# Kernel optimization log

Hardware: AMD Instinct MI355X
Metric: run time of the kernel (lower is better)

## Reference

```python
import jax, jax.numpy as jnp
import numpy as np

F_FRAMES = 128   # number of frames (seq_start_end rows)
P_PEDS = 32      # pedestrians per frame (uniform)
B = F_FRAMES * P_PEDS
E, H, BN, PM, M = 64, 128, 1024, 512, 1024
PRED_LEN = 12


def setup_inputs() -> dict:
    key = jax.random.key(0)
    ks = jax.random.split(key, 20)
    n = lambda k, s, sc=0.05: (jax.random.normal(k, s) * sc).astype(jnp.float32)
    starts = jnp.arange(F_FRAMES, dtype=jnp.int32) * P_PEDS
    seq_start_end = jnp.stack([starts, starts + P_PEDS], axis=1)
    return {
        "h0": n(ks[0], (1, B, H), 1.0),
        "c0": n(ks[1], (1, B, H), 1.0),
        "obs_final_pos": n(ks[2], (B, 2), 1.0),
        "obs_final_pos_rel": n(ks[3], (B, 2), 1.0),
        "W_emb": n(ks[4], (2, E)), "b_emb": jnp.zeros((E,), jnp.float32),
        "W_ih": n(ks[5], (4 * H, E)), "W_hh": n(ks[6], (4 * H, H)),
        "b_ih": jnp.zeros((4 * H,), jnp.float32), "b_hh": jnp.zeros((4 * H,), jnp.float32),
        "W_pos": n(ks[7], (H, 2)), "b_pos": jnp.zeros((2,), jnp.float32),
        "W_pe": n(ks[8], (2, E)), "b_pe": jnp.zeros((E,), jnp.float32),
        "W_p1": n(ks[9], (E + H, PM)), "b_p1": jnp.zeros((PM,), jnp.float32),
        "W_p2": n(ks[10], (PM, BN)), "b_p2": jnp.zeros((BN,), jnp.float32),
        "W_m1": n(ks[11], (H + BN, M)), "b_m1": jnp.zeros((M,), jnp.float32),
        "W_m2": n(ks[12], (M, H)), "b_m2": jnp.zeros((H,), jnp.float32),
        "seq_start_end": seq_start_end,
    }


def reference(h0, c0, obs_final_pos, obs_final_pos_rel,
              W_emb, b_emb, W_ih, W_hh, b_ih, b_hh, W_pos, b_pos,
              W_pe, b_pe, W_p1, b_p1, W_p2, b_p2, W_m1, b_m1, W_m2, b_m2,
              seq_start_end):
    Bn = h0.shape[1]
    F = seq_start_end.shape[0]
    P = Bn // F  # uniform frame size
    h, c = h0[0], c0[0]
    x0 = obs_final_pos_rel @ W_emb + b_emb  # decoder input embedding

    def step(carry, _):
        x, h, c, last_pos = carry
        # LSTM cell (PyTorch gate order i,f,g,o)
        gates = x @ W_ih.T + h @ W_hh.T + b_ih + b_hh  # (B, 4H)
        i, f, g, o = jnp.split(gates, 4, axis=-1)
        i, f, o = jax.nn.sigmoid(i), jax.nn.sigmoid(f), jax.nn.sigmoid(o)
        c_new = f * c + i * jnp.tanh(g)
        h_new = o * jnp.tanh(c_new)
        rel_pos = h_new @ W_pos + b_pos
        curr_pos = rel_pos + last_pos
        # PoolNet: per-frame pairwise rel-pos embed + MLP + max over neighbours j
        pos = curr_pos.reshape(F, P, 2)
        hf = h_new.reshape(F, P, H)
        rel = pos[:, None, :, :] - pos[:, :, None, :]  # rel[f,i,j] = pos_j - pos_i
        e = rel @ W_pe + b_pe  # (F,P,P,E)
        feat = jnp.concatenate(
            [e, jnp.broadcast_to(hf[:, None], (F, P, P, H))], axis=-1)  # h of j
        z = jax.nn.relu(feat @ W_p1 + b_p1)
        z = jax.nn.relu(z @ W_p2 + b_p2)  # (F,P,P,BN)
        pool_h = z.max(axis=2).reshape(Bn, BN)
        # hidden refresh MLP
        mi = jnp.concatenate([h_new, pool_h], axis=-1)
        nh = jax.nn.relu(mi @ W_m1 + b_m1)
        nh = jax.nn.relu(nh @ W_m2 + b_m2)
        x_new = rel_pos @ W_emb + b_emb
        return (x_new, nh, c_new, curr_pos), (curr_pos, rel_pos)

    _, (pred_seq, pred_seq_rel) = jax.lax.scan(
        jax.checkpoint(step), (x0, h, c, obs_final_pos), None, length=PRED_LEN)
    return pred_seq, pred_seq_rel
```

## Files before the change

### kernel.cpp

```cpp
#include <hip/hip_runtime.h>

#define NB 4096
#define HD 128
#define ED 64
#define NF 128
#define NP 32
#define TSTEPS 12

typedef __attribute__((ext_vector_type(8))) short short8;
typedef __attribute__((ext_vector_type(8))) __bf16 bf16x8;
typedef __attribute__((ext_vector_type(8))) _Float16 f16x8;
typedef __attribute__((ext_vector_type(4))) float f32x4;

#define MFMA16(a, b, c) __builtin_amdgcn_mfma_f32_16x16x32_bf16((a), (b), (c), 0, 0, 0)
#define MFMAH(a, b, c)  __builtin_amdgcn_mfma_f32_16x16x32_f16((a), (b), (c), 0, 0, 0)

__device__ __forceinline__ unsigned short f2bf(float f) {
  unsigned int x = __float_as_uint(f);
  x += 0x7fffu + ((x >> 16) & 1u);
  return (unsigned short)(x >> 16);
}

__device__ __forceinline__ float sigm(float x) { return 1.0f / (1.0f + expf(-x)); }

__device__ __forceinline__ f16x8 relu8(f16x8 x) {
  return __builtin_elementwise_max(x, (f16x8)(_Float16)0);
}


__global__ __launch_bounds__(256) void k_transpose_bf(const float* __restrict__ W,
                                                      unsigned short* __restrict__ Wt,
                                                      int K, int N) {
  __shared__ float t[32][33];
  int nb = blockIdx.x * 32, kb = blockIdx.y * 32;
  int tx = threadIdx.x & 31, ty = threadIdx.x >> 5;
  #pragma unroll
  for (int r = 0; r < 32; r += 8)
    t[ty + r][tx] = W[(size_t)(kb + ty + r) * N + nb + tx];
  __syncthreads();
  #pragma unroll
  for (int r = 0; r < 32; r += 8)
    Wt[(size_t)(nb + ty + r) * K + kb + tx] = f2bf(t[tx][ty + r]);
}

__global__ __launch_bounds__(256) void k_transpose_f16(const float* __restrict__ W,
                                                       _Float16* __restrict__ Wt,
                                                       int K, int N) {
  __shared__ float t[32][33];
  int nb = blockIdx.x * 32, kb = blockIdx.y * 32;
  int tx = threadIdx.x & 31, ty = threadIdx.x >> 5;
  #pragma unroll
  for (int r = 0; r < 32; r += 8)
    t[ty + r][tx] = W[(size_t)(kb + ty + r) * N + nb + tx];
  __syncthreads();
  #pragma unroll
  for (int r = 0; r < 32; r += 8)
    Wt[(size_t)(nb + ty + r) * K + kb + tx] = (_Float16)t[tx][ty + r];
}

__global__ __launch_bounds__(256) void k_pack_lstm_w(const float* __restrict__ Wih,
                                                     const float* __restrict__ Whh,
                                                     float* __restrict__ WihT,
                                                     float* __restrict__ WhhT) {
  int idx = blockIdx.x * 256 + threadIdx.x;
  if (idx < 64 * 512) { int k = idx >> 9, n = idx & 511; WihT[idx] = Wih[n * 64 + k]; }
  if (idx < 128 * 512) { int k = idx >> 9, n = idx & 511; WhhT[idx] = Whh[n * 128 + k]; }
}

__global__ __launch_bounds__(256) void k_pack_wpp(const float* __restrict__ Wpe,
                                                  const float* __restrict__ bpe,
                                                  const float* __restrict__ Wp1,
                                                  const float* __restrict__ bp1,
                                                  float* __restrict__ Wpp,
                                                  float* __restrict__ cvec) {
  int n = blockIdx.x * 256 + threadIdx.x;
  if (n >= 512) return;
  float s0 = 0.f, s1 = 0.f, sc = 0.f;
  for (int k = 0; k < 64; ++k) {
    float w = Wp1[k * 512 + n];
    s0 += Wpe[k] * w;
    s1 += Wpe[64 + k] * w;
    sc += bpe[k] * w;
  }
  Wpp[n * 2] = s0; Wpp[n * 2 + 1] = s1; cvec[n] = sc + bp1[n];
}

__global__ __launch_bounds__(256) void k_x0(const float* __restrict__ ofr,
                                            const float* __restrict__ Wemb,
                                            const float* __restrict__ bemb,
                                            float* __restrict__ x) {
  int idx = blockIdx.x * 256 + threadIdx.x;
  if (idx >= NB * ED) return;
  int row = idx >> 6, e = idx & 63;
  x[idx] = bemb[e] + ofr[row * 2] * Wemb[e] + ofr[row * 2 + 1] * Wemb[64 + e];
}


__global__ __launch_bounds__(256) void k12_lstm_uv(
    const float* __restrict__ x, const float* __restrict__ hin, const float* __restrict__ cin,
    const float* __restrict__ WihT, const float* __restrict__ WhhT,
    const float* __restrict__ bih, const float* __restrict__ bhh,
    const float* __restrict__ Wpos, const float* __restrict__ bpos,
    const float* __restrict__ Wemb, const float* __restrict__ bemb,
    const float* __restrict__ lastpos,
    const float* __restrict__ Wp1, const float* __restrict__ Wpp,
    const float* __restrict__ cvec,
    float* __restrict__ cout, unsigned short* __restrict__ mi,
    float* __restrict__ posout, float* __restrict__ xout,
    float* __restrict__ outc, float* __restrict__ outr,
    _Float16* __restrict__ u16, _Float16* __restrict__ v16) {
  __shared__ float xh[8][192];
  __shared__ float hnl[8][128];
  __shared__ float rp[8][2];
  __shared__ float cp[8][2];
  int tid = threadIdx.x;
  int r0 = blockIdx.x * 8;
  for (int idx = tid; idx < 8 * 192; idx += 256) {
    int r = idx / 192, k = idx % 192;
    xh[r][k] = (k < 64) ? x[(r0 + r) * 64 + k] : hin[(r0 + r) * 128 + (k - 64)];
  }
  __syncthreads();
  int j = tid & 127, rg = tid >> 7;
  float acc0[4], acc1[4], acc2[4], acc3[4];
  {
    float b0 = bih[j] + bhh[j];
    float b1 = bih[128 + j] + bhh[128 + j];
    float b2 = bih[256 + j] + bhh[256 + j];
    float b3 = bih[384 + j] + bhh[384 + j];
    #pragma unroll
    for (int r = 0; r < 4; ++r) { acc0[r] = b0; acc1[r] = b1; acc2[r] = b2; acc3[r] = b3; }
  }
  for (int k = 0; k < 64; ++k) {
    float w0 = WihT[k * 512 + j], w1 = WihT[k * 512 + 128 + j],
          w2 = WihT[k * 512 + 256 + j], w3 = WihT[k * 512 + 384 + j];
    #pragma unroll
    for (int r = 0; r < 4; ++r) {
      float xv = xh[rg * 4 + r][k];
      acc0[r] += w0 * xv; acc1[r] += w1 * xv; acc2[r] += w2 * xv; acc3[r] += w3 * xv;
    }
  }
  for (int k = 0; k < 128; ++k) {
    float w0 = WhhT[k * 512 + j], w1 = WhhT[k * 512 + 128 + j],
          w2 = WhhT[k * 512 + 256 + j], w3 = WhhT[k * 512 + 384 + j];
    #pragma unroll
    for (int r = 0; r < 4; ++r) {
      float hv = xh[rg * 4 + r][64 + k];
      acc0[r] += w0 * hv; acc1[r] += w1 * hv; acc2[r] += w2 * hv; acc3[r] += w3 * hv;
    }
  }
  #pragma unroll
  for (int r = 0; r < 4; ++r) {
    int row = r0 + rg * 4 + r;
    float ig = sigm(acc0[r]), fg = sigm(acc1[r]), gg = tanhf(acc2[r]), og = sigm(acc3[r]);
    float cn = fg * cin[row * 128 + j] + ig * gg;
    float hv = og * tanhf(cn);
    cout[row * 128 + j] = cn;
    mi[(size_t)row * 1152 + j] = f2bf(hv);
    hnl[rg * 4 + r][j] = hv;
  }
  __syncthreads();
  {
    int r = tid >> 5;
    int d = (tid >> 4) & 1;
    int l = tid & 15;
    float s = 0.f;
    #pragma unroll
    for (int k = l; k < 128; k += 16) s += hnl[r][k] * Wpos[k * 2 + d];
    s += __shfl_xor(s, 1);
    s += __shfl_xor(s, 2);
    s += __shfl_xor(s, 4);
    s += __shfl_xor(s, 8);
    if (l == 0) {
      int row = r0 + r;
      float rel = s + bpos[d];
      float cur = rel + lastpos[row * 2 + d];
      rp[r][d] = rel;
      cp[r][d] = cur;
      posout[row * 2 + d] = cur;
      outc[row * 2 + d] = cur;
      outr[row * 2 + d] = rel;
    }
  }
  __syncthreads();
  for (int idx = tid; idx < 8 * 64; idx += 256) {
    int r = idx >> 6, e = idx & 63;
    xout[(r0 + r) * 64 + e] = bemb[e] + rp[r][0] * Wemb[e] + rp[r][1] * Wemb[64 + e];
  }
  int n = tid, n2 = tid + 256;
  float aA[8], aB[8];
  #pragma unroll
  for (int r = 0; r < 8; ++r) { aA[r] = 0.f; aB[r] = 0.f; }
  for (int k = 0; k < 128; ++k) {
    float wA = Wp1[(64 + k) * 512 + n], wB = Wp1[(64 + k) * 512 + n2];
    #pragma unroll
    for (int r = 0; r < 8; ++r) { aA[r] += wA * hnl[r][k]; aB[r] += wB * hnl[r][k]; }
  }
  float wp0A = Wpp[n * 2], wp1A = Wpp[n * 2 + 1], cA = cvec[n];
  float wp0B = Wpp[n2 * 2], wp1B = Wpp[n2 * 2 + 1], cB = cvec[n2];
  #pragma unroll
  for (int r = 0; r < 8; ++r) {
    int row = r0 + r;
    float t0 = cp[r][0] * wp0A + cp[r][1] * wp1A;
    v16[(size_t)row * 512 + n] = (_Float16)t0;
    u16[(size_t)row * 512 + n] = (_Float16)(t0 + aA[r] + cA);
    float t1 = cp[r][0] * wp0B + cp[r][1] * wp1B;
    v16[(size_t)row * 512 + n2] = (_Float16)t1;
    u16[(size_t)row * 512 + n2] = (_Float16)(t1 + aB[r] + cB);
  }
}

__global__ __launch_bounds__(256, 2) void k3_pool(
    const _Float16* __restrict__ u16, const _Float16* __restrict__ v16,
    const _Float16* __restrict__ Bt, const float* __restrict__ bp2,
    unsigned short* __restrict__ mi) {
  __shared__ _Float16 v_lds[4 * 512];
  __shared__ _Float16 u_ch[2][32 * 32];
  __shared__ _Float16 b_ch[2][256 * 32];
  int f = blockIdx.x, ig = blockIdx.y, ng = blockIdx.z;
  int tid = threadIdx.x, wid = tid >> 6, lane = tid & 63;
  int c = lane & 15, q = lane >> 4;
  int ip = wid >> 1, nh = wid & 1;

  int srow = tid >> 2, sseg = tid & 3;
  const _Float16* gB = Bt + (size_t)(ng * 256 + srow) * 512 + sseg * 8;
  const _Float16* gU = u16 + (size_t)(f * 32 + srow) * 512 + sseg * 8;
  int lOff = srow * 32 + sseg * 8;

  {
    int vr = tid >> 6, vs = tid & 63;
    *(f16x8*)(v_lds + vr * 512 + vs * 8) =
        *(const f16x8*)(v16 + (size_t)(f * 32 + ig * 4 + vr) * 512 + vs * 8);
  }
  #pragma unroll
  for (int t = 0; t < 4; ++t)
    *(f16x8*)(b_ch[0] + lOff + t * 64 * 32) = *(const f16x8*)(gB + (size_t)t * 64 * 512);
  if (tid < 128) *(f16x8*)(u_ch[0] + lOff) = *(const f16x8*)(gU);
  __syncthreads();

  f32x4 acc[2][2][8];
  #pragma unroll
  for (int a = 0; a < 2; ++a)
    #pragma unroll
    for (int b = 0; b < 2; ++b)
      #pragma unroll
      for (int n = 0; n < 8; ++n) acc[a][b][n] = (f32x4){0.f, 0.f, 0.f, 0.f};

  const _Float16* vb0 = v_lds + (ip * 2 + 0) * 512 + q * 8;
  const _Float16* vb1 = v_lds + (ip * 2 + 1) * 512 + q * 8;
  int uoff0 = c * 32 + q * 8;
  int uoff1 = (16 + c) * 32 + q * 8;
  int boff = (nh * 128 + c) * 32 + q * 8;

  #pragma unroll 2
  for (int ks = 0; ks < 16; ++ks) {
    int cur = ks & 1;
    f16x8 rB0, rB1, rB2, rB3, rU;
    if (ks < 15) {
      const _Float16* g = gB + (size_t)(ks + 1) * 32;
      rB0 = *(const f16x8*)(g);
      rB1 = *(const f16x8*)(g + (size_t)64 * 512);
      rB2 = *(const f16x8*)(g + (size_t)128 * 512);
      rB3 = *(const f16x8*)(g + (size_t)192 * 512);
      if (tid < 128) rU = *(const f16x8*)(gU + (size_t)(ks + 1) * 32);
    }
    const _Float16* ub = u_ch[cur];
    const _Float16* bb = b_ch[cur];
    f16x8 uf0 = *(const f16x8*)(ub + uoff0);
    f16x8 uf1 = *(const f16x8*)(ub + uoff1);
    f16x8 vv0 = *(const f16x8*)(vb0 + ks * 32);
    f16x8 vv1 = *(const f16x8*)(vb1 + ks * 32);
    f16x8 a00 = relu8(uf0 - vv0), a01 = relu8(uf1 - vv0);
    f16x8 a10 = relu8(uf0 - vv1), a11 = relu8(uf1 - vv1);
    __builtin_amdgcn_s_setprio(1);
    #pragma unroll
    for (int nt = 0; nt < 8; ++nt) {
      f16x8 bf = *(const f16x8*)(bb + boff + nt * 16 * 32);
      acc[0][0][nt] = MFMAH(a00, bf, acc[0][0][nt]);
      acc[0][1][nt] = MFMAH(a01, bf, acc[0][1][nt]);
      acc[1][0][nt] = MFMAH(a10, bf, acc[1][0][nt]);
      acc[1][1][nt] = MFMAH(a11, bf, acc[1][1][nt]);
    }
    __builtin_amdgcn_s_setprio(0);
    if (ks < 15) {
      _Float16* lb = b_ch[cur ^ 1] + lOff;
      *(f16x8*)(lb) = rB0;
      *(f16x8*)(lb + 64 * 32) = rB1;
      *(f16x8*)(lb + 128 * 32) = rB2;
      *(f16x8*)(lb + 192 * 32) = rB3;
      if (tid < 128) *(f16x8*)(u_ch[cur ^ 1] + lOff) = rU;
    }
    __syncthreads();
  }

  int colbase = ng * 256 + nh * 128;
  #pragma unroll
  for (int ii = 0; ii < 2; ++ii) {
    int rowg = f * 32 + ig * 4 + ip * 2 + ii;
    #pragma unroll
    for (int nt = 0; nt < 8; ++nt) {
      f32x4 x0 = acc[ii][0][nt], x1 = acc[ii][1][nt];
      float m = fmaxf(fmaxf(fmaxf(x0[0], x0[1]), fmaxf(x0[2], x0[3])),
                      fmaxf(fmaxf(x1[0], x1[1]), fmaxf(x1[2], x1[3])));
      m = fmaxf(m, __shfl_xor(m, 16));
      m = fmaxf(m, __shfl_xor(m, 32));
      if (q == 0) {
        int col = colbase + nt * 16 + c;
        float val = fmaxf(m + bp2[col], 0.f);
        mi[(size_t)rowg * 1152 + 128 + col] = f2bf(val);
      }
    }
  }
}

__global__ __launch_bounds__(512) void k4_mlp1(
    const unsigned short* __restrict__ mi, const unsigned short* __restrict__ Wt,
    const float* __restrict__ bm1, unsigned short* __restrict__ nh1) {
  int bid = blockIdx.x;
  int mb = bid & 63, nb = bid >> 6;
  int tid = threadIdx.x, wid = tid >> 6, lane = tid & 63;
  int row0 = mb * 64 + (wid >> 2) * 32;
  int nc0 = nb * 256 + (wid & 3) * 64;
  int c = lane & 15, q = lane >> 4;
  const unsigned short* a0p = mi + (size_t)(row0 + c) * 1152;
  const unsigned short* a1p = a0p + 16 * 1152;
  const unsigned short* bb = Wt + (size_t)(nc0 + c) * 1152;
  f32x4 acc[2][4];
  #pragma unroll
  for (int a = 0; a < 2; ++a)
    #pragma unroll
    for (int b = 0; b < 4; ++b) acc[a][b] = (f32x4){0.f, 0.f, 0.f, 0.f};
  for (int ks = 0; ks < 36; ++ks) {
    int k0 = ks * 32 + q * 8;
    bf16x8 a0 = *(const bf16x8*)(a0p + k0);
    bf16x8 a1 = *(const bf16x8*)(a1p + k0);
    #pragma unroll
    for (int nt = 0; nt < 4; ++nt) {
      bf16x8 bf = *(const bf16x8*)(bb + (size_t)nt * 16 * 1152 + k0);
      acc[0][nt] = MFMA16(a0, bf, acc[0][nt]);
      acc[1][nt] = MFMA16(a1, bf, acc[1][nt]);
    }
  }
  #pragma unroll
  for (int mt = 0; mt < 2; ++mt)
    #pragma unroll
    for (int nt = 0; nt < 4; ++nt)
      #pragma unroll
      for (int r = 0; r < 4; ++r) {
        int row = row0 + mt * 16 + q * 4 + r;
        int col = nc0 + nt * 16 + c;
        float val = fmaxf(acc[mt][nt][r] + bm1[col], 0.f);
        nh1[(size_t)row * 1024 + col] = f2bf(val);
      }
}

__global__ __launch_bounds__(128) void k5_mlp2(
    const unsigned short* __restrict__ nh1, const unsigned short* __restrict__ Wt,
    const float* __restrict__ bm2, float* __restrict__ hout) {
  int bid = blockIdx.x;
  int tid = threadIdx.x, wid = tid >> 6, lane = tid & 63;
  int row0 = bid * 16;
  int nc0 = wid * 64;
  int c = lane & 15, q = lane >> 4;
  const unsigned short* ap = nh1 + (size_t)(row0 + c) * 1024;
  const unsigned short* bb = Wt + (size_t)(nc0 + c) * 1024;
  f32x4 acc[4];
  #pragma unroll
  for (int b = 0; b < 4; ++b) acc[b] = (f32x4){0.f, 0.f, 0.f, 0.f};
  for (int ks = 0; ks < 32; ++ks) {
    int k0 = ks * 32 + q * 8;
    bf16x8 a = *(const bf16x8*)(ap + k0);
    #pragma unroll
    for (int nt = 0; nt < 4; ++nt) {
      bf16x8 bf = *(const bf16x8*)(bb + (size_t)nt * 16 * 1024 + k0);
      acc[nt] = MFMA16(a, bf, acc[nt]);
    }
  }
  #pragma unroll
  for (int nt = 0; nt < 4; ++nt)
    #pragma unroll
    for (int r = 0; r < 4; ++r) {
      int row = row0 + q * 4 + r;
      int col = nc0 + nt * 16 + c;
      hout[(size_t)row * 128 + col] = fmaxf(acc[nt][r] + bm2[col], 0.f);
    }
}


extern "C" void kernel_launch(void* const* d_in, const int* in_sizes, int n_in,
                              void* d_out, int out_size, void* d_ws, size_t ws_size,
                              hipStream_t stream) {
  const float* h0   = (const float*)d_in[0];
  const float* c0   = (const float*)d_in[1];
  const float* ofp  = (const float*)d_in[2];
  const float* ofr  = (const float*)d_in[3];
  const float* Wemb = (const float*)d_in[4];
  const float* bemb = (const float*)d_in[5];
  const float* Wih  = (const float*)d_in[6];
  const float* Whh  = (const float*)d_in[7];
  const float* bih  = (const float*)d_in[8];
  const float* bhh  = (const float*)d_in[9];
  const float* Wpos = (const float*)d_in[10];
  const float* bpos = (const float*)d_in[11];
  const float* Wpe  = (const float*)d_in[12];
  const float* bpe  = (const float*)d_in[13];
  const float* Wp1  = (const float*)d_in[14];
  const float* bp1  = (const float*)d_in[15];
  const float* Wp2  = (const float*)d_in[16];
  const float* bp2  = (const float*)d_in[17];
  const float* Wm1  = (const float*)d_in[18];
  const float* bm1  = (const float*)d_in[19];
  const float* Wm2  = (const float*)d_in[20];
  const float* bm2  = (const float*)d_in[21];

  char* ws = (char*)d_ws;
  size_t off = 0;
  auto alloc = [&](size_t bytes) {
    char* p = ws + off;
    off += (bytes + 255) & ~(size_t)255;
    return p;
  };
  float* h    = (float*)alloc((size_t)NB * HD * 4);
  float* cst  = (float*)alloc((size_t)NB * HD * 4);
  float* xbuf = (float*)alloc((size_t)NB * ED * 4);
  float* pos  = (float*)alloc((size_t)NB * 2 * 4);
  _Float16* u16 = (_Float16*)alloc((size_t)NB * 512 * 2);
  _Float16* v16 = (_Float16*)alloc((size_t)NB * 512 * 2);
  unsigned short* mi   = (unsigned short*)alloc((size_t)NB * 1152 * 2);
  unsigned short* nh1  = (unsigned short*)alloc((size_t)NB * 1024 * 2);
  float* WihT = (float*)alloc(64 * 512 * 4);
  float* WhhT = (float*)alloc(128 * 512 * 4);
  float* Wpp  = (float*)alloc(512 * 2 * 4);
  float* cvec = (float*)alloc(512 * 4);
  _Float16* Bt2 = (_Float16*)alloc((size_t)1024 * 512 * 2);
  unsigned short* Wm1t = (unsigned short*)alloc((size_t)1024 * 1152 * 2);
  unsigned short* Wm2t = (unsigned short*)alloc((size_t)128 * 1024 * 2);

  float* outc = (float*)d_out;
  float* outr = outc + (size_t)TSTEPS * NB * 2;

  k_pack_lstm_w<<<256, 256, 0, stream>>>(Wih, Whh, WihT, WhhT);
  k_pack_wpp<<<2, 256, 0, stream>>>(Wpe, bpe, Wp1, bp1, Wpp, cvec);
  k_transpose_f16<<<dim3(1024 / 32, 512 / 32), 256, 0, stream>>>(Wp2, Bt2, 512, 1024);
  k_transpose_bf<<<dim3(1024 / 32, 1152 / 32), 256, 0, stream>>>(Wm1, Wm1t, 1152, 1024);
  k_transpose_bf<<<dim3(128 / 32, 1024 / 32), 256, 0, stream>>>(Wm2, Wm2t, 1024, 128);
  k_x0<<<NB * ED / 256, 256, 0, stream>>>(ofr, Wemb, bemb, xbuf);

  for (int t = 0; t < TSTEPS; ++t) {
    const float* hin = (t == 0) ? h0 : h;
    const float* cin = (t == 0) ? c0 : cst;
    const float* lp  = (t == 0) ? ofp : pos;
    k12_lstm_uv<<<NB / 8, 256, 0, stream>>>(xbuf, hin, cin, WihT, WhhT, bih, bhh,
                                            Wpos, bpos, Wemb, bemb, lp, Wp1, Wpp, cvec,
                                            cst, mi, pos, xbuf,
                                            outc + (size_t)t * NB * 2,
                                            outr + (size_t)t * NB * 2, u16, v16);
    k3_pool<<<dim3(128, 8, 4), 256, 0, stream>>>(u16, v16, Bt2, bp2, mi);
    k4_mlp1<<<256, 512, 0, stream>>>(mi, Wm1t, bm1, nh1);
    k5_mlp2<<<256, 128, 0, stream>>>(nh1, Wm2t, bm2, h);
  }
}
```

Before: 2.983 ms.

## Prepack W_p2 into MFMA fragment order and stream B directly into registers

W_p2 is now prepacked into MFMA B-fragment order, so each lane loads its B operand straight from global memory into registers, double-buffered one k-step ahead. The full 32-row u tile is staged once into XOR-swizzled LDS, which removes the per-k-step LDS staging and the __syncthreads from the pool kernel's main loop. The cost is that B loads per wave now come from global/L2 without LDS sharing between waves, plus higher register pressure from holding 16 f16x8 B fragments.

```diff
diff --git a/kernel.cpp b/kernel.cpp
--- a/kernel.cpp
+++ b/kernel.cpp
@@ -43,19 +43,16 @@
     Wt[(size_t)(nb + ty + r) * K + kb + tx] = f2bf(t[tx][ty + r]);
 }
 
-__global__ __launch_bounds__(256) void k_transpose_f16(const float* __restrict__ W,
-                                                       _Float16* __restrict__ Wt,
-                                                       int K, int N) {
-  __shared__ float t[32][33];
-  int nb = blockIdx.x * 32, kb = blockIdx.y * 32;
-  int tx = threadIdx.x & 31, ty = threadIdx.x >> 5;
-  #pragma unroll
-  for (int r = 0; r < 32; r += 8)
-    t[ty + r][tx] = W[(size_t)(kb + ty + r) * N + nb + tx];
-  __syncthreads();
-  #pragma unroll
-  for (int r = 0; r < 32; r += 8)
-    Wt[(size_t)(nb + ty + r) * K + kb + tx] = (_Float16)t[tx][ty + r];
+__global__ __launch_bounds__(256) void k_pack_bfrag(const float* __restrict__ Wp2,
+                                                    _Float16* __restrict__ Bf) {
+  int U = blockIdx.x * 256 + threadIdx.x;
+  int l = U & 63, cb = (U >> 6) & 63, ks = U >> 12;
+  int col = cb * 16 + (l & 15);
+  int k0 = ks * 32 + (l >> 4) * 8;
+  f16x8 r;
+  #pragma unroll
+  for (int e = 0; e < 8; ++e) r[e] = (_Float16)Wp2[(size_t)(k0 + e) * 1024 + col];
+  *(f16x8*)(Bf + (size_t)U * 8) = r;
 }
 
 __global__ __launch_bounds__(256) void k_pack_lstm_w(const float* __restrict__ Wih,
@@ -211,30 +208,37 @@
 
 __global__ __launch_bounds__(256, 2) void k3_pool(
     const _Float16* __restrict__ u16, const _Float16* __restrict__ v16,
-    const _Float16* __restrict__ Bt, const float* __restrict__ bp2,
+    const _Float16* __restrict__ Bf, const float* __restrict__ bp2,
     unsigned short* __restrict__ mi) {
+  __shared__ _Float16 u_lds[32 * 512];
   __shared__ _Float16 v_lds[4 * 512];
-  __shared__ _Float16 u_ch[2][32 * 32];
-  __shared__ _Float16 b_ch[2][256 * 32];
   int f = blockIdx.x, ig = blockIdx.y, ng = blockIdx.z;
   int tid = threadIdx.x, wid = tid >> 6, lane = tid & 63;
   int c = lane & 15, q = lane >> 4;
   int ip = wid >> 1, nh = wid & 1;
 
-  int srow = tid >> 2, sseg = tid & 3;
-  const _Float16* gB = Bt + (size_t)(ng * 256 + srow) * 512 + sseg * 8;
-  const _Float16* gU = u16 + (size_t)(f * 32 + srow) * 512 + sseg * 8;
-  int lOff = srow * 32 + sseg * 8;
-
+  const f16x8* Bfu = (const f16x8*)Bf;
+  int cb0 = ng * 16 + nh * 8;
+
+  f16x8 B0[8], B1[8];
+  #pragma unroll
+  for (int nt = 0; nt < 8; ++nt)
+    B0[nt] = Bfu[(size_t)((cb0 + nt) * 64 + lane)];
+
+  #pragma unroll
+  for (int t = 0; t < 8; ++t) {
+    int unit = tid + t * 256;
+    int row = unit >> 6, seg = unit & 63;
+    f16x8 val = *(const f16x8*)(u16 + (size_t)(f * 32 + row) * 512 + seg * 8);
+    int byte = (row << 10) + (seg << 4);
+    byte ^= (row & 7) << 4;
+    *(f16x8*)((char*)u_lds + byte) = val;
+  }
   {
-    int vr = tid >> 6, vs = tid & 63;
-    *(f16x8*)(v_lds + vr * 512 + vs * 8) =
-        *(const f16x8*)(v16 + (size_t)(f * 32 + ig * 4 + vr) * 512 + vs * 8);
-  }
-  #pragma unroll
-  for (int t = 0; t < 4; ++t)
-    *(f16x8*)(b_ch[0] + lOff + t * 64 * 32) = *(const f16x8*)(gB + (size_t)t * 64 * 512);
-  if (tid < 128) *(f16x8*)(u_ch[0] + lOff) = *(const f16x8*)(gU);
+    int row = tid >> 6, seg = tid & 63;
+    *(f16x8*)(v_lds + (row << 9) + seg * 8) =
+        *(const f16x8*)(v16 + (size_t)(f * 32 + ig * 4 + row) * 512 + seg * 8);
+  }
   __syncthreads();
 
   f32x4 acc[2][2][8];
@@ -245,51 +249,37 @@
       #pragma unroll
       for (int n = 0; n < 8; ++n) acc[a][b][n] = (f32x4){0.f, 0.f, 0.f, 0.f};
 
-  const _Float16* vb0 = v_lds + (ip * 2 + 0) * 512 + q * 8;
-  const _Float16* vb1 = v_lds + (ip * 2 + 1) * 512 + q * 8;
-  int uoff0 = c * 32 + q * 8;
-  int uoff1 = (16 + c) * 32 + q * 8;
-  int boff = (nh * 128 + c) * 32 + q * 8;
-
-  #pragma unroll 2
+  int ub0 = (c << 10) + (q << 4);
+  int usw = (c & 7) << 4;
+  const _Float16* vp0 = v_lds + ((ip * 2 + 0) << 9) + q * 8;
+  const _Float16* vp1 = vp0 + 512;
+
+  #pragma unroll
   for (int ks = 0; ks < 16; ++ks) {
-    int cur = ks & 1;
-    f16x8 rB0, rB1, rB2, rB3, rU;
     if (ks < 15) {
-      const _Float16* g = gB + (size_t)(ks + 1) * 32;
-      rB0 = *(const f16x8*)(g);
-      rB1 = *(const f16x8*)(g + (size_t)64 * 512);
-      rB2 = *(const f16x8*)(g + (size_t)128 * 512);
-      rB3 = *(const f16x8*)(g + (size_t)192 * 512);
-      if (tid < 128) rU = *(const f16x8*)(gU + (size_t)(ks + 1) * 32);
-    }
-    const _Float16* ub = u_ch[cur];
-    const _Float16* bb = b_ch[cur];
-    f16x8 uf0 = *(const f16x8*)(ub + uoff0);
-    f16x8 uf1 = *(const f16x8*)(ub + uoff1);
-    f16x8 vv0 = *(const f16x8*)(vb0 + ks * 32);
-    f16x8 vv1 = *(const f16x8*)(vb1 + ks * 32);
+      #pragma unroll
+      for (int nt = 0; nt < 8; ++nt)
+        B1[nt] = Bfu[(size_t)(((ks + 1) * 64 + cb0 + nt) * 64 + lane)];
+    }
+    int kb = ks << 6;
+    f16x8 uf0 = *(const f16x8*)((const char*)u_lds + ((ub0 + kb) ^ usw));
+    f16x8 uf1 = *(const f16x8*)((const char*)u_lds + ((ub0 + 16384 + kb) ^ usw));
+    f16x8 vv0 = *(const f16x8*)(vp0 + ks * 32);
+    f16x8 vv1 = *(const f16x8*)(vp1 + ks * 32);
     f16x8 a00 = relu8(uf0 - vv0), a01 = relu8(uf1 - vv0);
     f16x8 a10 = relu8(uf0 - vv1), a11 = relu8(uf1 - vv1);
     __builtin_amdgcn_s_setprio(1);
     #pragma unroll
     for (int nt = 0; nt < 8; ++nt) {
-      f16x8 bf = *(const f16x8*)(bb + boff + nt * 16 * 32);
+      f16x8 bf = B0[nt];
       acc[0][0][nt] = MFMAH(a00, bf, acc[0][0][nt]);
       acc[0][1][nt] = MFMAH(a01, bf, acc[0][1][nt]);
       acc[1][0][nt] = MFMAH(a10, bf, acc[1][0][nt]);
       acc[1][1][nt] = MFMAH(a11, bf, acc[1][1][nt]);
     }
     __builtin_amdgcn_s_setprio(0);
-    if (ks < 15) {
-      _Float16* lb = b_ch[cur ^ 1] + lOff;
-      *(f16x8*)(lb) = rB0;
-      *(f16x8*)(lb + 64 * 32) = rB1;
-      *(f16x8*)(lb + 128 * 32) = rB2;
-      *(f16x8*)(lb + 192 * 32) = rB3;
-      if (tid < 128) *(f16x8*)(u_ch[cur ^ 1] + lOff) = rU;
-    }
-    __syncthreads();
+    #pragma unroll
+    for (int nt = 0; nt < 8; ++nt) B0[nt] = B1[nt];
   }
 
   int colbase = ng * 256 + nh * 128;
@@ -431,7 +421,7 @@
   float* WhhT = (float*)alloc(128 * 512 * 4);
   float* Wpp  = (float*)alloc(512 * 2 * 4);
   float* cvec = (float*)alloc(512 * 4);
-  _Float16* Bt2 = (_Float16*)alloc((size_t)1024 * 512 * 2);
+  _Float16* Bf  = (_Float16*)alloc((size_t)1024 * 512 * 2);
   unsigned short* Wm1t = (unsigned short*)alloc((size_t)1024 * 1152 * 2);
   unsigned short* Wm2t = (unsigned short*)alloc((size_t)128 * 1024 * 2);
 
@@ -440,7 +430,7 @@
 
   k_pack_lstm_w<<<256, 256, 0, stream>>>(Wih, Whh, WihT, WhhT);
   k_pack_wpp<<<2, 256, 0, stream>>>(Wpe, bpe, Wp1, bp1, Wpp, cvec);
-  k_transpose_f16<<<dim3(1024 / 32, 512 / 32), 256, 0, stream>>>(Wp2, Bt2, 512, 1024);
+  k_pack_bfrag<<<256, 256, 0, stream>>>(Wp2, Bf);
   k_transpose_bf<<<dim3(1024 / 32, 1152 / 32), 256, 0, stream>>>(Wm1, Wm1t, 1152, 1024);
   k_transpose_bf<<<dim3(128 / 32, 1024 / 32), 256, 0, stream>>>(Wm2, Wm2t, 1024, 128);
   k_x0<<<NB * ED / 256, 256, 0, stream>>>(ofr, Wemb, bemb, xbuf);
@@ -454,7 +444,7 @@
                                             cst, mi, pos, xbuf,
                                             outc + (size_t)t * NB * 2,
                                             outr + (size_t)t * NB * 2, u16, v16);
-    k3_pool<<<dim3(128, 8, 4), 256, 0, stream>>>(u16, v16, Bt2, bp2, mi);
+    k3_pool<<<dim3(128, 8, 4), 256, 0, stream>>>(u16, v16, Bf, bp2, mi);
     k4_mlp1<<<256, 512, 0, stream>>>(mi, Wm1t, bm1, nh1);
     k5_mlp2<<<256, 128, 0, stream>>>(nh1, Wm2t, bm2, h);
   }
```

Result: faster. 2.723 ms (-8.7%).
